# Performance work log

Measured on AMD Instinct MI355X. Metric: run time of the kernel, lower is better.

Reference implementation:

```python
import jax, jax.numpy as jnp
import numpy as np

B, N, C = 4, 4096, 16
HID, HEADS, OUT = 64, 4, 64
NEG = -1e16

def setup_inputs() -> dict:
    key = jax.random.key(0)
    ks = jax.random.split(key, 7)
    x = jax.random.normal(ks[0], (B, N, C), dtype=jnp.float32)
    # sparse-ish binary adjacency with self-loops, stored dense as in the torch module
    graph = (jax.random.randint(ks[1], (N, N), 0, 2)).astype(jnp.float32)
    graph = jnp.maximum(graph, jnp.eye(N, dtype=jnp.float32))
    # per-head Linear weights (bias=False) and the per-layer bias parameter b
    Ws = jax.random.normal(ks[2], (HEADS, C, HID), dtype=jnp.float32)   # W.weight.T per head
    bs = jax.random.normal(ks[3], (HEADS, HID), dtype=jnp.float32)
    W_out = jax.random.normal(ks[4], (HEADS * HID, OUT), dtype=jnp.float32)
    b_out = jax.random.normal(ks[5], (OUT,), dtype=jnp.float32)
    return {"x": x, "graph": graph, "Ws": Ws, "bs": bs, "W_out": W_out, "b_out": b_out}

def _gat_layer(x, graph, W, b):
    # x: [B,N,Cin], W: [Cin,D], b: [D]
    h = jnp.einsum('bnc,cd->bnd', x, W)                      # [B,N,D]
    s = jnp.einsum('bnd,bmd->bnm', h, h) * graph[None]       # [B,N,N]
    s = jnp.where(s == 0.0, NEG, s)                          # masked_fill(eq 0, -1e16)
    attn = jax.nn.softmax(s, axis=2)
    return jnp.einsum('bnm,bmd->bnd', attn, h) + b

def _leaky_relu(x):
    return jnp.where(x >= 0, x, 0.2 * x)

def reference(x, graph, Ws, bs, W_out, b_out):
    # multi-head layers, concatenated on feature dim (head-major)
    heads = jax.vmap(lambda W, b: _gat_layer(x, graph, W, b))(Ws, bs)  # [H,B,N,D]
    cat = jnp.transpose(heads, (1, 2, 0, 3)).reshape(B, N, HEADS * HID)
    cat = _leaky_relu(cat)
    out = _gat_layer(cat, graph, W_out, b_out)
    return _leaky_relu(out)
```

## Files before the change

kernel.cpp:

```cpp
#include <hip/hip_runtime.h>

typedef unsigned short u16;
typedef unsigned int u32;
typedef unsigned long long u64;
typedef __attribute__((ext_vector_type(8))) short bf16x8;
typedef __attribute__((ext_vector_type(4))) float f32x4;
typedef __attribute__((ext_vector_type(16))) float f32x16;

#define NEGF  -1.0e38f
#define MINIT -1.0e30f
#define LOG2E 1.4426950408889634f

__device__ __forceinline__ u16 f2bf(float x) {
  union { float f; u32 u; } v; v.f = x;
  u32 r = v.u + 0x7fffu + ((v.u >> 16) & 1u);
  return (u16)(r >> 16);
}
__device__ __forceinline__ float bf2f(u16 b) {
  union { u32 u; float f; } v; v.u = ((u32)b) << 16;
  return v.f;
}
__device__ __forceinline__ float leaky(float x) { return x >= 0.f ? x : 0.2f * x; }

__device__ __forceinline__ void gload16(const void* g, void* l) {
  __builtin_amdgcn_global_load_lds(
      (const __attribute__((address_space(1))) u32*)(unsigned long long)g,
      (__attribute__((address_space(3))) u32*)(u32)(unsigned long long)l,
      16, 0, 0);
}

__global__ __launch_bounds__(256) void pack_kernel(const float* __restrict__ graph,
                                                   u64* __restrict__ bits) {
  const int n = blockIdx.x;
  const int w = threadIdx.x >> 6, lane = threadIdx.x & 63;
  const float* gr = graph + (size_t)n * 4096;
  for (int j = 0; j < 16; ++j) {
    const int wd = j * 4 + w;
    u64 m = __ballot(gr[wd * 64 + lane] != 0.0f);
    if (lane == 0) bits[(size_t)n * 64 + wd] = m;
  }
}

__global__ __launch_bounds__(256) void h1_kernel(const float* __restrict__ x,
                                                 const float* __restrict__ Ws,
                                                 u16* __restrict__ h1a, u16* __restrict__ h1b,
                                                 u16* __restrict__ h1c) {
  const int blk = blockIdx.x;
  const int h = threadIdx.x >> 6, d = threadIdx.x & 63;
  const float* xr = x + (size_t)blk * 16;
  const float* Wp = Ws + h * (16 * 64) + d;
  float acc = 0.f;
  #pragma unroll
  for (int c = 0; c < 16; ++c) acc += xr[c] * Wp[c * 64];
  const int b = blk >> 12, n = blk & 4095;
  const size_t o = ((size_t)(b * 4 + h) * 4096 + n) * 64 + d;
  u16 a = f2bf(acc);
  float r1 = acc - bf2f(a);
  u16 bq = f2bf(r1);
  float r2 = r1 - bf2f(bq);
  h1a[o] = a; h1b[o] = bq; h1c[o] = f2bf(r2);
}

__global__ __launch_bounds__(256) void transpose_kernel(const u16* __restrict__ src,
                                                        u16* __restrict__ dst) {
  const int p = blockIdx.y, n0 = blockIdx.x * 64;
  const u16* s = src + (size_t)p * 4096 * 64;
  u16* d = dst + (size_t)p * 4096 * 64;
  __shared__ u16 tile[64][66];
  const int col = threadIdx.x & 63, r4 = threadIdx.x >> 6;
  #pragma unroll
  for (int i = 0; i < 16; ++i) {
    const int r = i * 4 + r4;
    tile[r][col] = s[(size_t)(n0 + r) * 64 + col];
  }
  __syncthreads();
  const int cs = (col & 51) | ((col & 4) << 1) | ((col & 8) >> 1);
  #pragma unroll
  for (int i = 0; i < 16; ++i) {
    const int r = i * 4 + r4;
    d[(size_t)r * 4096 + n0 + cs] = tile[col][r];
  }
}

__global__ __launch_bounds__(256) void h2_kernel(const float* __restrict__ cat,
                                                 const float* __restrict__ Wout,
                                                 u16* __restrict__ h2a, u16* __restrict__ h2b,
                                                 u16* __restrict__ h2c) {
  const int row = blockIdx.x * 4 + (threadIdx.x >> 6);
  const int d = threadIdx.x & 63;
  const float* cr = cat + (size_t)row * 256;
  float acc = 0.f;
  for (int c4 = 0; c4 < 64; ++c4) {
    const float4 cv = *(const float4*)(cr + c4 * 4);
    acc += cv.x * Wout[(c4 * 4 + 0) * 64 + d];
    acc += cv.y * Wout[(c4 * 4 + 1) * 64 + d];
    acc += cv.z * Wout[(c4 * 4 + 2) * 64 + d];
    acc += cv.w * Wout[(c4 * 4 + 3) * 64 + d];
  }
  const size_t o = (size_t)row * 64 + d;
  u16 a = f2bf(acc);
  float r1 = acc - bf2f(a);
  u16 bq = f2bf(r1);
  float r2 = r1 - bf2f(bq);
  h2a[o] = a; h2b[o] = bq; h2c[o] = f2bf(r2);
}

template <int LAYER>
__global__ __launch_bounds__(256) void attn_kernel(
    const u16* __restrict__ Ha, const u16* __restrict__ Hb, const u16* __restrict__ Hc,
    const u16* __restrict__ HaT, const u16* __restrict__ HbT,
    const u64* __restrict__ bits, const float* __restrict__ bias,
    float* __restrict__ outp, float* __restrict__ pm, float* __restrict__ pl) {
  constexpr int NCH = (LAYER == 1) ? 64 : 16;
  const int orig = blockIdx.x + 32 * blockIdx.y;
  const int sid = (orig & 7) * 64 + (orig >> 3);
  const int bx = sid & 31;
  const int py = sid >> 5;
  const int pass = (LAYER == 1) ? py : (py & 3);
  const int chg0 = (LAYER == 1) ? 0 : ((py >> 2) * 16);

  const int t = threadIdx.x;
  const int wq = t >> 6;
  const int lane = t & 63;
  const int c = lane & 31;
  const int g1 = lane >> 5;
  const int qbase = bx * 128 + wq * 32;
  const int q = qbase + c;
  const size_t poffb = (size_t)pass * (4096 * 64) * 2;

  __shared__ f32x4 smem_v[3584];
  char* smem = (char*)smem_v;

  const int srow = lane >> 3;
  const int scol = ((lane & 7) ^ srow) << 4;
  const char* gKa = (const char*)Ha + poffb;
  const char* gKb = (const char*)Hb + poffb;
  const char* gKc = (const char*)Hc + poffb;
  const char* gVa = (const char*)HaT + poffb;
  const char* gVb = (const char*)HbT + poffb;

  auto stageK = [&](int chg) {
    const size_t cb = (size_t)chg * 8192;
    #pragma unroll
    for (int ii = 0; ii < 2; ++ii) {
      const int r0 = wq * 16 + ii * 8;
      const size_t so = cb + (size_t)(r0 + srow) * 128 + scol;
      const int dofs = r0 * 128;
      gload16(gKa + so, smem + 0     + dofs);
      gload16(gKb + so, smem + 8192  + dofs);
      gload16(gKc + so, smem + 16384 + dofs);
    }
  };
  auto stageV = [&](int chg, int buf) {
    const char* gsrc = (wq >> 1) ? gVb : gVa;
    char* dbase = smem + 24576 + buf * 16384 + (wq >> 1) * 8192;
    const size_t cb = (size_t)chg * 128;
    #pragma unroll
    for (int ii = 0; ii < 4; ++ii) {
      const int r0 = (wq & 1) * 32 + ii * 8;
      const size_t so = cb + (size_t)(r0 + srow) * 8192 + scol;
      gload16(gsrc + so, dbase + r0 * 128);
    }
  };

  bf16x8 qf[3][4];
  {
    const char* qra = (const char*)Ha + poffb + (size_t)q * 128 + 16 * g1;
    const char* qrb = (const char*)Hb + poffb + (size_t)q * 128 + 16 * g1;
    const char* qrc = (const char*)Hc + poffb + (size_t)q * 128 + 16 * g1;
    #pragma unroll
    for (int kk = 0; kk < 4; ++kk) {
      qf[0][kk] = *(const bf16x8*)(qra + kk * 32);
      qf[1][kk] = *(const bf16x8*)(qrb + kk * 32);
      qf[2][kk] = *(const bf16x8*)(qrc + kk * 32);
    }
  }

  const u64* bqp = bits + (size_t)q * 64;

  const int swz = (c & 7) << 4;
  int iK[4];
  #pragma unroll
  for (int kk = 0; kk < 4; ++kk) iK[kk] = c * 128 + ((32 * kk + 16 * g1) ^ swz);

  f32x16 Of0, Of1;
  #pragma unroll
  for (int r = 0; r < 16; ++r) { Of0[r] = 0.f; Of1[r] = 0.f; }
  float mrow = MINIT, lrow = 0.f;

  stageK(chg0);
  stageV(chg0, 0);
  u64 mcur = bqp[chg0];
  __syncthreads();

  #pragma unroll 1
  for (int ch = 0; ch < NCH; ++ch) {
    const int chg = chg0 + ch;
    __builtin_amdgcn_sched_barrier(0);
    f32x16 s0, s1;
    #pragma unroll
    for (int r = 0; r < 16; ++r) { s0[r] = 0.f; s1[r] = 0.f; }
    __builtin_amdgcn_s_setprio(1);
    #pragma unroll
    for (int kk = 0; kk < 4; ++kk) {
      #pragma unroll
      for (int mt = 0; mt < 2; ++mt) {
        const char* kp = smem + mt * 4096 + iK[kk];
        const bf16x8 ka = *(const bf16x8*)(kp);
        const bf16x8 kb = *(const bf16x8*)(kp + 8192);
        const bf16x8 kc = *(const bf16x8*)(kp + 16384);
        f32x16& sa = mt ? s1 : s0;
        sa = __builtin_amdgcn_mfma_f32_32x32x16_bf16(ka, qf[2][kk], sa, 0, 0, 0);
        sa = __builtin_amdgcn_mfma_f32_32x32x16_bf16(kb, qf[1][kk], sa, 0, 0, 0);
        sa = __builtin_amdgcn_mfma_f32_32x32x16_bf16(kc, qf[0][kk], sa, 0, 0, 0);
        sa = __builtin_amdgcn_mfma_f32_32x32x16_bf16(ka, qf[1][kk], sa, 0, 0, 0);
        sa = __builtin_amdgcn_mfma_f32_32x32x16_bf16(kb, qf[0][kk], sa, 0, 0, 0);
        sa = __builtin_amdgcn_mfma_f32_32x32x16_bf16(ka, qf[0][kk], sa, 0, 0, 0);
      }
    }
    __builtin_amdgcn_s_setprio(0);
    __builtin_amdgcn_sched_barrier(0);
    __builtin_amdgcn_s_barrier();
    __builtin_amdgcn_sched_barrier(0);
    if (ch + 1 < NCH) {
      stageK(chg + 1);
      stageV(chg + 1, (ch + 1) & 1);
    }
    __builtin_amdgcn_sched_barrier(0);

    const u32 a0 = (u32)(mcur >> (4 * g1));
    const u32 a1 = (u32)(mcur >> (32 + 4 * g1));
    #pragma unroll
    for (int r = 0; r < 16; ++r) {
      const int off = (r & 3) + 8 * (r >> 2);
      s0[r] = ((a0 >> off) & 1u) ? s0[r] : NEGF;
      s1[r] = ((a1 >> off) & 1u) ? s1[r] : NEGF;
    }
    float m8[8];
    #pragma unroll
    for (int j = 0; j < 8; ++j)
      m8[j] = fmaxf(fmaxf(s0[2*j], s0[2*j+1]), fmaxf(s1[2*j], s1[2*j+1]));
    float mm = fmaxf(fmaxf(fmaxf(m8[0], m8[1]), fmaxf(m8[2], m8[3])),
                     fmaxf(fmaxf(m8[4], m8[5]), fmaxf(m8[6], m8[7])));
    mm = fmaxf(mm, __shfl_xor(mm, 32));
    if (!__all(mm <= mrow + 8.f)) {
      const float mn = fmaxf(mrow, mm);
      const float scl = exp2f((mrow - mn) * LOG2E);
      #pragma unroll
      for (int r = 0; r < 16; ++r) { Of0[r] *= scl; Of1[r] *= scl; }
      lrow *= scl;
      mrow = mn;
    }
    #pragma unroll
    for (int r = 0; r < 16; ++r) {
      s0[r] = exp2f((s0[r] - mrow) * LOG2E);
      s1[r] = exp2f((s1[r] - mrow) * LOG2E);
    }
    {
      float r4[4];
      #pragma unroll
      for (int j = 0; j < 4; ++j)
        r4[j] = ((s0[4*j] + s0[4*j+1]) + (s0[4*j+2] + s0[4*j+3]))
              + ((s1[4*j] + s1[4*j+1]) + (s1[4*j+2] + s1[4*j+3]));
      float rs = (r4[0] + r4[1]) + (r4[2] + r4[3]);
      rs += __shfl_xor(rs, 32);
      lrow += rs;
    }

    bf16x8 pa[4], pb[4];
    #pragma unroll
    for (int kk = 0; kk < 4; ++kk) {
      const f32x16& sm = (kk >> 1) ? s1 : s0;
      const int rb = 8 * (kk & 1);
      union { u32 w[4]; bf16x8 v; } ua, ub;
      #pragma unroll
      for (int j = 0; j < 4; ++j) {
        const float p0 = sm[rb + 2*j], p1 = sm[rb + 2*j + 1];
        const u16 h0 = f2bf(p0), h1 = f2bf(p1);
        ua.w[j] = (u32)h0 | ((u32)h1 << 16);
        const u16 l0 = f2bf(p0 - bf2f(h0));
        const u16 l1 = f2bf(p1 - bf2f(h1));
        ub.w[j] = (u32)l0 | ((u32)l1 << 16);
      }
      pa[kk] = ua.v; pb[kk] = ub.v;
    }

    const char* vbase = smem + 24576 + (ch & 1) * 16384;
    __builtin_amdgcn_s_setprio(1);
    #pragma unroll
    for (int dt = 0; dt < 2; ++dt) {
      f32x16& o = dt ? Of1 : Of0;
      #pragma unroll
      for (int kk = 0; kk < 4; ++kk) {
        const char* vp = vbase + dt * 4096 + iK[kk];
        const bf16x8 va = *(const bf16x8*)(vp);
        const bf16x8 vb = *(const bf16x8*)(vp + 8192);
        o = __builtin_amdgcn_mfma_f32_32x32x16_bf16(vb, pb[kk], o, 0, 0, 0);
        o = __builtin_amdgcn_mfma_f32_32x32x16_bf16(va, pb[kk], o, 0, 0, 0);
        o = __builtin_amdgcn_mfma_f32_32x32x16_bf16(vb, pa[kk], o, 0, 0, 0);
        o = __builtin_amdgcn_mfma_f32_32x32x16_bf16(va, pa[kk], o, 0, 0, 0);
      }
    }
    __builtin_amdgcn_s_setprio(0);

    u64 mnxt = 0;
    if (ch + 1 < NCH) mnxt = bqp[chg + 1];
    __builtin_amdgcn_sched_barrier(0);
    if (ch + 1 < NCH) {
      asm volatile("s_waitcnt vmcnt(1)" ::: "memory");
    } else {
      asm volatile("s_waitcnt vmcnt(0)" ::: "memory");
    }
    __builtin_amdgcn_sched_barrier(0);
    __builtin_amdgcn_s_barrier();
    mcur = mnxt;
  }

  char* reg = smem + wq * 8704;
  const float inv = (LAYER == 1) ? (1.0f / lrow) : 1.0f;
  #pragma unroll
  for (int dt = 0; dt < 2; ++dt) {
    const f32x16& o = dt ? Of1 : Of0;
    #pragma unroll
    for (int i = 0; i < 4; ++i) {
      f32x4 v;
      v[0] = o[4*i+0] * inv; v[1] = o[4*i+1] * inv;
      v[2] = o[4*i+2] * inv; v[3] = o[4*i+3] * inv;
      *(f32x4*)(reg + c * 272 + (32 * dt + 8 * i + 4 * g1) * 4) = v;
    }
  }
  if (LAYER == 2 && lane < 32) {
    pm[(size_t)py * 4096 + q] = mrow;
    pl[(size_t)py * 4096 + q] = lrow;
  }
  __syncthreads();
  const int d0 = (lane & 15) * 4;
  const float* bp = (LAYER == 1) ? (bias + (pass & 3) * 64) : bias;
  #pragma unroll
  for (int qq = 0; qq < 8; ++qq) {
    const int ql = qq * 4 + (lane >> 4);
    f32x4 v = *(const f32x4*)(reg + ql * 272 + (lane & 15) * 16);
    const int qg = qbase + ql;
    if (LAYER == 1) {
      v[0] = leaky(v[0] + bp[d0 + 0]);
      v[1] = leaky(v[1] + bp[d0 + 1]);
      v[2] = leaky(v[2] + bp[d0 + 2]);
      v[3] = leaky(v[3] + bp[d0 + 3]);
      *(f32x4*)&outp[((size_t)((pass >> 2) * 4096 + qg)) * 256 + (pass & 3) * 64 + d0] = v;
    } else {
      *(f32x4*)&outp[((size_t)py * 4096 + qg) * 64 + d0] = v;
    }
  }
}

__global__ __launch_bounds__(256) void merge_kernel(
    const float* __restrict__ pO, const float* __restrict__ pm, const float* __restrict__ pl,
    const float* __restrict__ bo, float* __restrict__ dout) {
  const int t = threadIdx.x;
  const int d = t & 63;
  const int q = blockIdx.x * 4 + (t >> 6);
  const int pass = blockIdx.y;
  float m[4], l[4], o[4];
  #pragma unroll
  for (int s = 0; s < 4; ++s) {
    const size_t idx = (size_t)(s * 4 + pass) * 4096 + q;
    m[s] = pm[idx]; l[s] = pl[idx];
    o[s] = pO[idx * 64 + d];
  }
  const float M = fmaxf(fmaxf(m[0], m[1]), fmaxf(m[2], m[3]));
  float num = 0.f, den = 0.f;
  #pragma unroll
  for (int s = 0; s < 4; ++s) {
    const float w = exp2f((m[s] - M) * LOG2E);
    num += w * o[s]; den += w * l[s];
  }
  const float r = num / den + bo[d];
  dout[((size_t)pass * 4096 + q) * 64 + d] = leaky(r);
}

extern "C" void kernel_launch(void* const* d_in, const int* in_sizes, int n_in,
                              void* d_out, int out_size, void* d_ws, size_t ws_size,
                              hipStream_t stream) {
  const float* x     = (const float*)d_in[0];
  const float* graph = (const float*)d_in[1];
  const float* Ws    = (const float*)d_in[2];
  const float* bs    = (const float*)d_in[3];
  const float* W_out = (const float*)d_in[4];
  const float* b_out = (const float*)d_in[5];
  char* ws = (char*)d_ws;
  const size_t MiB = 1048576;

  u64* bits   = (u64*)(ws + 0 * MiB);
  u16* h1a    = (u16*)(ws + 2 * MiB);
  u16* h1b    = (u16*)(ws + 10 * MiB);
  u16* h1c    = (u16*)(ws + 18 * MiB);
  u16* h1aT   = (u16*)(ws + 26 * MiB);
  u16* h1bT   = (u16*)(ws + 34 * MiB);
  float* catb = (float*)(ws + 42 * MiB);
  u16* h2a    = (u16*)(ws + 58 * MiB);
  u16* h2b    = (u16*)(ws + 60 * MiB);
  u16* h2c    = (u16*)(ws + 62 * MiB);
  u16* h2aT   = (u16*)(ws + 64 * MiB);
  u16* h2bT   = (u16*)(ws + 66 * MiB);
  float* pO   = (float*)(ws + 2 * MiB);
  float* pmb  = (float*)(ws + 18 * MiB);
  float* plb  = (float*)(ws + 18 * MiB + 262144);

  pack_kernel<<<4096, 256, 0, stream>>>(graph, bits);
  h1_kernel<<<16384, 256, 0, stream>>>(x, Ws, h1a, h1b, h1c);
  transpose_kernel<<<dim3(64, 16), 256, 0, stream>>>(h1a, h1aT);
  transpose_kernel<<<dim3(64, 16), 256, 0, stream>>>(h1b, h1bT);
  attn_kernel<1><<<dim3(32, 16), 256, 0, stream>>>(h1a, h1b, h1c, h1aT, h1bT,
                                                   bits, bs, catb, nullptr, nullptr);
  h2_kernel<<<4096, 256, 0, stream>>>(catb, W_out, h2a, h2b, h2c);
  transpose_kernel<<<dim3(64, 4), 256, 0, stream>>>(h2a, h2aT);
  transpose_kernel<<<dim3(64, 4), 256, 0, stream>>>(h2b, h2bT);
  attn_kernel<2><<<dim3(32, 16), 256, 0, stream>>>(h2a, h2b, h2c, h2aT, h2bT,
                                                   bits, b_out, pO, pmb, plb);
  merge_kernel<<<dim3(1024, 4), 256, 0, stream>>>(pO, pmb, plb, b_out, (float*)d_out);
}
```

Baseline: 502.2 us.

## Split attention key range across more blocks, single-buffer V, drop one MFMA term

Layer-1 attention now splits the key range in two, and layer-2 splits it in eight instead of four. Each split writes partial max, sum and output, and a generic merge kernel combines them and applies bias and leaky ReLU. The grid doubles to 1024 blocks, launch bounds request 4 blocks per SM, and V staging becomes single-buffered with extra barriers so LDS shrinks and occupancy can rise. The PV product also drops the low-times-low bf16 term, reducing MFMA work at a small precision cost, and the extra merge pass adds global traffic.

New measurement: 702.3 us. 1.4x slower.

```diff
diff --git a/kernel.cpp b/kernel.cpp
--- a/kernel.cpp
+++ b/kernel.cpp
@@ -105,19 +105,18 @@
   h2a[o] = a; h2b[o] = bq; h2c[o] = f2bf(r2);
 }
 
-template <int LAYER>
-__global__ __launch_bounds__(256) void attn_kernel(
+template <int NCH, int PSHIFT>
+__global__ __launch_bounds__(256, 4) void attn_kernel(
     const u16* __restrict__ Ha, const u16* __restrict__ Hb, const u16* __restrict__ Hc,
     const u16* __restrict__ HaT, const u16* __restrict__ HbT,
-    const u64* __restrict__ bits, const float* __restrict__ bias,
-    float* __restrict__ outp, float* __restrict__ pm, float* __restrict__ pl) {
-  constexpr int NCH = (LAYER == 1) ? 64 : 16;
+    const u64* __restrict__ bits,
+    float* __restrict__ pO, float* __restrict__ pm, float* __restrict__ pl) {
   const int orig = blockIdx.x + 32 * blockIdx.y;
-  const int sid = (orig & 7) * 64 + (orig >> 3);
+  const int sid = (orig & 7) * 128 + (orig >> 3);
   const int bx = sid & 31;
   const int py = sid >> 5;
-  const int pass = (LAYER == 1) ? py : (py & 3);
-  const int chg0 = (LAYER == 1) ? 0 : ((py >> 2) * 16);
+  const int pass = py & ((1 << PSHIFT) - 1);
+  const int chg0 = (py >> PSHIFT) * NCH;
 
   const int t = threadIdx.x;
   const int wq = t >> 6;
@@ -128,7 +127,7 @@
   const int q = qbase + c;
   const size_t poffb = (size_t)pass * (4096 * 64) * 2;
 
-  __shared__ f32x4 smem_v[3584];
+  __shared__ f32x4 smem_v[2560];
   char* smem = (char*)smem_v;
 
   const int srow = lane >> 3;
@@ -151,9 +150,9 @@
       gload16(gKc + so, smem + 16384 + dofs);
     }
   };
-  auto stageV = [&](int chg, int buf) {
+  auto stageV = [&](int chg) {
     const char* gsrc = (wq >> 1) ? gVb : gVa;
-    char* dbase = smem + 24576 + buf * 16384 + (wq >> 1) * 8192;
+    char* dbase = smem + 24576 + (wq >> 1) * 8192;
     const size_t cb = (size_t)chg * 128;
     #pragma unroll
     for (int ii = 0; ii < 4; ++ii) {
@@ -189,8 +188,9 @@
   float mrow = MINIT, lrow = 0.f;
 
   stageK(chg0);
-  stageV(chg0, 0);
+  stageV(chg0);
   u64 mcur = bqp[chg0];
+  asm volatile("s_waitcnt vmcnt(0)" ::: "memory");
   __syncthreads();
 
   #pragma unroll 1
@@ -224,8 +224,9 @@
     __builtin_amdgcn_sched_barrier(0);
     if (ch + 1 < NCH) {
       stageK(chg + 1);
-      stageV(chg + 1, (ch + 1) & 1);
-    }
+    }
+    u64 mnxt = 0;
+    if (ch + 1 < NCH) mnxt = bqp[chg + 1];
     __builtin_amdgcn_sched_barrier(0);
 
     const u32 a0 = (u32)(mcur >> (4 * g1));
@@ -285,7 +286,16 @@
       pa[kk] = ua.v; pb[kk] = ub.v;
     }
 
-    const char* vbase = smem + 24576 + (ch & 1) * 16384;
+    __builtin_amdgcn_sched_barrier(0);
+    if (ch + 1 < NCH) {
+      asm volatile("s_waitcnt vmcnt(7)" ::: "memory");
+    } else {
+      asm volatile("s_waitcnt vmcnt(0)" ::: "memory");
+    }
+    __builtin_amdgcn_sched_barrier(0);
+    __builtin_amdgcn_s_barrier();
+
+    const char* vbase = smem + 24576;
     __builtin_amdgcn_s_setprio(1);
     #pragma unroll
     for (int dt = 0; dt < 2; ++dt) {
@@ -295,87 +305,80 @@
         const char* vp = vbase + dt * 4096 + iK[kk];
         const bf16x8 va = *(const bf16x8*)(vp);
         const bf16x8 vb = *(const bf16x8*)(vp + 8192);
-        o = __builtin_amdgcn_mfma_f32_32x32x16_bf16(vb, pb[kk], o, 0, 0, 0);
+        o = __builtin_amdgcn_mfma_f32_32x32x16_bf16(vb, pa[kk], o, 0, 0, 0);
         o = __builtin_amdgcn_mfma_f32_32x32x16_bf16(va, pb[kk], o, 0, 0, 0);
-        o = __builtin_amdgcn_mfma_f32_32x32x16_bf16(vb, pa[kk], o, 0, 0, 0);
         o = __builtin_amdgcn_mfma_f32_32x32x16_bf16(va, pa[kk], o, 0, 0, 0);
       }
     }
     __builtin_amdgcn_s_setprio(0);
-
-    u64 mnxt = 0;
-    if (ch + 1 < NCH) mnxt = bqp[chg + 1];
+    __builtin_amdgcn_sched_barrier(0);
+    __builtin_amdgcn_s_barrier();
     __builtin_amdgcn_sched_barrier(0);
     if (ch + 1 < NCH) {
-      asm volatile("s_waitcnt vmcnt(1)" ::: "memory");
-    } else {
-      asm volatile("s_waitcnt vmcnt(0)" ::: "memory");
-    }
-    __builtin_amdgcn_sched_barrier(0);
+      stageV(chg + 1);
+      __builtin_amdgcn_sched_barrier(0);
+      asm volatile("s_waitcnt vmcnt(4)" ::: "memory");
+      __builtin_amdgcn_sched_barrier(0);
+    }
     __builtin_amdgcn_s_barrier();
     mcur = mnxt;
   }
 
   char* reg = smem + wq * 8704;
-  const float inv = (LAYER == 1) ? (1.0f / lrow) : 1.0f;
   #pragma unroll
   for (int dt = 0; dt < 2; ++dt) {
     const f32x16& o = dt ? Of1 : Of0;
     #pragma unroll
     for (int i = 0; i < 4; ++i) {
       f32x4 v;
-      v[0] = o[4*i+0] * inv; v[1] = o[4*i+1] * inv;
-      v[2] = o[4*i+2] * inv; v[3] = o[4*i+3] * inv;
+      v[0] = o[4*i+0]; v[1] = o[4*i+1];
+      v[2] = o[4*i+2]; v[3] = o[4*i+3];
       *(f32x4*)(reg + c * 272 + (32 * dt + 8 * i + 4 * g1) * 4) = v;
     }
   }
-  if (LAYER == 2 && lane < 32) {
+  if (lane < 32) {
     pm[(size_t)py * 4096 + q] = mrow;
     pl[(size_t)py * 4096 + q] = lrow;
   }
   __syncthreads();
   const int d0 = (lane & 15) * 4;
-  const float* bp = (LAYER == 1) ? (bias + (pass & 3) * 64) : bias;
   #pragma unroll
   for (int qq = 0; qq < 8; ++qq) {
     const int ql = qq * 4 + (lane >> 4);
     f32x4 v = *(const f32x4*)(reg + ql * 272 + (lane & 15) * 16);
     const int qg = qbase + ql;
-    if (LAYER == 1) {
-      v[0] = leaky(v[0] + bp[d0 + 0]);
-      v[1] = leaky(v[1] + bp[d0 + 1]);
-      v[2] = leaky(v[2] + bp[d0 + 2]);
-      v[3] = leaky(v[3] + bp[d0 + 3]);
-      *(f32x4*)&outp[((size_t)((pass >> 2) * 4096 + qg)) * 256 + (pass & 3) * 64 + d0] = v;
-    } else {
-      *(f32x4*)&outp[((size_t)py * 4096 + qg) * 64 + d0] = v;
-    }
-  }
-}
-
+    *(f32x4*)&pO[((size_t)py * 4096 + qg) * 64 + d0] = v;
+  }
+}
+
+template <int NS, int NP, bool CAT>
 __global__ __launch_bounds__(256) void merge_kernel(
-    const float* __restrict__ pO, const float* __restrict__ pm, const float* __restrict__ pl,
-    const float* __restrict__ bo, float* __restrict__ dout) {
+    const float* __restrict__ pO, const float* __restrict__ pm,
+    const float* __restrict__ pl, const float* __restrict__ bias,
+    float* __restrict__ out) {
   const int t = threadIdx.x;
   const int d = t & 63;
   const int q = blockIdx.x * 4 + (t >> 6);
   const int pass = blockIdx.y;
-  float m[4], l[4], o[4];
-  #pragma unroll
-  for (int s = 0; s < 4; ++s) {
-    const size_t idx = (size_t)(s * 4 + pass) * 4096 + q;
-    m[s] = pm[idx]; l[s] = pl[idx];
-    o[s] = pO[idx * 64 + d];
-  }
-  const float M = fmaxf(fmaxf(m[0], m[1]), fmaxf(m[2], m[3]));
+  float m[NS];
+  float M = MINIT;
+  #pragma unroll
+  for (int s = 0; s < NS; ++s) {
+    m[s] = pm[(size_t)(s * NP + pass) * 4096 + q];
+    M = fmaxf(M, m[s]);
+  }
   float num = 0.f, den = 0.f;
   #pragma unroll
-  for (int s = 0; s < 4; ++s) {
+  for (int s = 0; s < NS; ++s) {
+    const size_t idx = (size_t)(s * NP + pass) * 4096 + q;
     const float w = exp2f((m[s] - M) * LOG2E);
-    num += w * o[s]; den += w * l[s];
-  }
-  const float r = num / den + bo[d];
-  dout[((size_t)pass * 4096 + q) * 64 + d] = leaky(r);
+    num += w * pO[idx * 64 + d];
+    den += w * pl[idx];
+  }
+  float r = num / den + (CAT ? bias[(pass & 3) * 64 + d] : bias[d]);
+  r = leaky(r);
+  if (CAT) out[((size_t)(pass >> 2) * 4096 + q) * 256 + (pass & 3) * 64 + d] = r;
+  else     out[((size_t)pass * 4096 + q) * 64 + d] = r;
 }
 
 extern "C" void kernel_launch(void* const* d_in, const int* in_sizes, int n_in,
@@ -402,20 +405,21 @@
   u16* h2c    = (u16*)(ws + 62 * MiB);
   u16* h2aT   = (u16*)(ws + 64 * MiB);
   u16* h2bT   = (u16*)(ws + 66 * MiB);
-  float* pO   = (float*)(ws + 2 * MiB);
-  float* pmb  = (float*)(ws + 18 * MiB);
-  float* plb  = (float*)(ws + 18 * MiB + 262144);
+  float* pO   = (float*)(ws + 68 * MiB);
+  float* pmb  = (float*)(ws + 100 * MiB);
+  float* plb  = (float*)(ws + 100 * MiB + 524288);
 
   pack_kernel<<<4096, 256, 0, stream>>>(graph, bits);
   h1_kernel<<<16384, 256, 0, stream>>>(x, Ws, h1a, h1b, h1c);
   transpose_kernel<<<dim3(64, 16), 256, 0, stream>>>(h1a, h1aT);
   transpose_kernel<<<dim3(64, 16), 256, 0, stream>>>(h1b, h1bT);
-  attn_kernel<1><<<dim3(32, 16), 256, 0, stream>>>(h1a, h1b, h1c, h1aT, h1bT,
-                                                   bits, bs, catb, nullptr, nullptr);
+  attn_kernel<32, 4><<<dim3(32, 32), 256, 0, stream>>>(h1a, h1b, h1c, h1aT, h1bT,
+                                                       bits, pO, pmb, plb);
+  merge_kernel<2, 16, true><<<dim3(1024, 16), 256, 0, stream>>>(pO, pmb, plb, bs, catb);
   h2_kernel<<<4096, 256, 0, stream>>>(catb, W_out, h2a, h2b, h2c);
   transpose_kernel<<<dim3(64, 4), 256, 0, stream>>>(h2a, h2aT);
   transpose_kernel<<<dim3(64, 4), 256, 0, stream>>>(h2b, h2bT);
-  attn_kernel<2><<<dim3(32, 16), 256, 0, stream>>>(h2a, h2b, h2c, h2aT, h2bT,
-                                                   bits, b_out, pO, pmb, plb);
-  merge_kernel<<<dim3(1024, 4), 256, 0, stream>>>(pO, pmb, plb, b_out, (float*)d_out);
-}
+  attn_kernel<8, 2><<<dim3(32, 32), 256, 0, stream>>>(h2a, h2b, h2c, h2aT, h2bT,
+                                                      bits, pO, pmb, plb);
+  merge_kernel<8, 4, false><<<dim3(1024, 4), 256, 0, stream>>>(pO, pmb, plb, b_out, (float*)d_out);
+}
```
